# Kernel tuning notes

Hardware: AMD Instinct MI355X
Metric: run time of the kernel (lower is better)

The kernel has to match this reference:

```python
import jax, jax.numpy as jnp
import numpy as np

N_NODES = 100000


def sage_conv(x, src, dst, W_l, b_l, W_r):
    # PyG SAGEConv (aggr='mean'): out = lin_l(mean_{j->i} x_j) + lin_r(x_i)
    # lin_l has bias, lin_r does not.
    msgs = x[src]                                             # [E, d_in] irregular gather
    summed = jax.ops.segment_sum(msgs, dst, num_segments=N_NODES)
    deg = jax.ops.segment_sum(jnp.ones((src.shape[0],), x.dtype), dst,
                              num_segments=N_NODES)
    mean = summed / jnp.maximum(deg, 1.0)[:, None]            # [N, d_in]
    return mean @ W_l.T + b_l + x @ W_r.T                     # [N, d_out]


def setup_inputs() -> dict:
    key = jax.random.key(0)
    ks = jax.random.split(key, 8)
    input_dim, hidden_dim, output_dim = 64, 128, 64
    E = 1600000
    x = jax.random.normal(ks[0], (N_NODES, input_dim), dtype=jnp.float32)
    edge_index = jax.random.randint(ks[1], (2, E), 0, N_NODES, dtype=jnp.int64)

    def glorot(k, shape):
        lim = (6.0 / (shape[0] + shape[1])) ** 0.5
        return jax.random.uniform(k, shape, jnp.float32, -lim, lim)

    W1_l = glorot(ks[2], (hidden_dim, input_dim))
    b1 = jnp.zeros((hidden_dim,), jnp.float32)
    W1_r = glorot(ks[3], (hidden_dim, input_dim))
    W2_l = glorot(ks[4], (output_dim, hidden_dim))
    b2 = jnp.zeros((output_dim,), jnp.float32)
    W2_r = glorot(ks[5], (output_dim, hidden_dim))
    return {"x": x, "edge_index": edge_index,
            "W1_l": W1_l, "b1": b1, "W1_r": W1_r,
            "W2_l": W2_l, "b2": b2, "W2_r": W2_r}


def reference(x, edge_index, W1_l, b1, W1_r, W2_l, b2, W2_r):
    src, dst = edge_index[0], edge_index[1]
    h = jax.nn.relu(sage_conv(x, src, dst, W1_l, b1, W1_r))
    h = jax.nn.relu(sage_conv(h, src, dst, W2_l, b2, W2_r))
    # Original module computes norm(x) and dropout(x) but discards the results,
    # so the returned value is just the second ReLU output.
    return h
```

## Files before the change

kernel.cpp:

```cpp
#include <hip/hip_runtime.h>
#include <hip/hip_bf16.h>


#define NODE_DIM0 64
#define NPBK 256
#define MAXB 512
#define CAPB 5120
#define EPB  4096
#define NSL  16

__device__ inline unsigned short f2bf(float f) {
    unsigned u = __float_as_uint(f);
    return (unsigned short)((u + 0x7fffu + ((u >> 16) & 1u)) >> 16);
}


__global__ __launch_bounds__(256) void bucket_scatter(const int* __restrict__ src,
                                                      const int* __restrict__ dst,
                                                      int* __restrict__ gcur,
                                                      unsigned* __restrict__ pairs, int E) {
    __shared__ int hist[MAXB];
    __shared__ int incl[MAXB];
    __shared__ int exoff[MAXB];
    __shared__ int cur[MAXB];
    __shared__ int chunkBase[MAXB];
    __shared__ unsigned staged[EPB];
    __shared__ unsigned short sbkt[EPB];
    const int t = threadIdx.x;
    const int base = blockIdx.x * EPB;
    int cnt = E - base; if (cnt > EPB) cnt = EPB;

    hist[t] = 0; hist[t + 256] = 0;
    __syncthreads();

    int myS[16], myD[16];
#pragma unroll
    for (int it = 0; it < 16; ++it) {
        int e = base + it * 256 + t;
        if (e < E) {
            myS[it] = src[e];
            myD[it] = dst[e];
            atomicAdd(&hist[myD[it] >> 8], 1);
        } else {
            myD[it] = -1;
        }
    }
    __syncthreads();

    incl[t] = hist[t]; incl[t + 256] = hist[t + 256];
    __syncthreads();
    for (int o = 1; o < MAXB; o <<= 1) {
        int a0 = (t >= o) ? incl[t - o] : 0;
        int a1 = (t + 256 >= o) ? incl[t + 256 - o] : 0;
        __syncthreads();
        incl[t] += a0; incl[t + 256] += a1;
        __syncthreads();
    }
    exoff[t] = incl[t] - hist[t];
    exoff[t + 256] = incl[t + 256] - hist[t + 256];
    cur[t] = 0; cur[t + 256] = 0;
    chunkBase[t] = (hist[t] > 0) ? atomicAdd(&gcur[t], hist[t]) : 0;
    chunkBase[t + 256] = (hist[t + 256] > 0) ? atomicAdd(&gcur[t + 256], hist[t + 256]) : 0;
    __syncthreads();

#pragma unroll
    for (int it = 0; it < 16; ++it) {
        if (myD[it] >= 0) {
            int b = myD[it] >> 8;
            int p = exoff[b] + atomicAdd(&cur[b], 1);
            staged[p] = ((unsigned)(myD[it] & (NPBK - 1)) << 17) | (unsigned)myS[it];
            sbkt[p] = (unsigned short)b;
        }
    }
    __syncthreads();

    for (int p = t; p < cnt; p += 256) {
        int b = sbkt[p];
        int g = chunkBase[b] + (p - exoff[b]);
        if (g < CAPB) pairs[(size_t)b * CAPB + g] = staged[p];
    }
}


__global__ __launch_bounds__(256) void bucket_csr(const unsigned* __restrict__ pairs,
                                                  const int* __restrict__ gcur,
                                                  int* __restrict__ startA,
                                                  int* __restrict__ degA,
                                                  int* __restrict__ esrc, int N) {
    __shared__ int ldeg[NPBK * NSL];
    __shared__ int lcur[NPBK * NSL];
    __shared__ int lsrc[CAPB];
    __shared__ int wsum[256];
    const int b = blockIdx.x;
    const int t = threadIdx.x;
    int cnt = gcur[b]; if (cnt > CAPB) cnt = CAPB;

    for (int i = t; i < NPBK * NSL; i += 256) ldeg[i] = 0;
    __syncthreads();

    const unsigned* reg = pairs + (size_t)b * CAPB;
    for (int i = t; i < cnt; i += 256) {
        unsigned w = reg[i];
        atomicAdd(&ldeg[((w >> 17) << 4) | ((w & 0x1FFFFu) >> 13)], 1);
    }
    __syncthreads();

    const int kbase = t * NSL;
    int run = 0, loc[NSL];
#pragma unroll
    for (int k = 0; k < NSL; ++k) { loc[k] = run; run += ldeg[kbase + k]; }
    wsum[t] = run;
    __syncthreads();
    for (int o = 1; o < 256; o <<= 1) {
        int add = (t >= o) ? wsum[t - o] : 0;
        __syncthreads();
        wsum[t] += add;
        __syncthreads();
    }
    const int excl = wsum[t] - run;
#pragma unroll
    for (int k = 0; k < NSL; ++k) lcur[kbase + k] = excl + loc[k];
    const int node0 = b * NPBK;
    if (node0 + t < N) { startA[node0 + t] = b * CAPB + excl; degA[node0 + t] = run; }
    __syncthreads();

    for (int i = t; i < cnt; i += 256) {
        unsigned w = reg[i];
        int key = (int)((w >> 17) << 4) | (int)((w & 0x1FFFFu) >> 13);
        int pos = atomicAdd(&lcur[key], 1);
        lsrc[pos] = (int)(w & 0x1FFFFu);
    }
    __syncthreads();

    int* outp = esrc + (size_t)b * CAPB;
    for (int i = t; i < cnt; i += 256) outp[i] = lsrc[i];
}


__global__ void cast_bf(const float* __restrict__ in, unsigned short* __restrict__ out,
                        int n4, int* __restrict__ gcur) {
    if (blockIdx.x == 0)
        for (int j = threadIdx.x; j < MAXB; j += 256) gcur[j] = 0;
    int i = blockIdx.x * 256 + threadIdx.x;
    if (i < n4) {
        float4 v = ((const float4*)in)[i];
        ushort4 o;
        o.x = f2bf(v.x); o.y = f2bf(v.y); o.z = f2bf(v.z); o.w = f2bf(v.w);
        ((ushort4*)out)[i] = o;
    }
}

__global__ void cast_weights(const float* __restrict__ a, const float* __restrict__ b,
                             const float* __restrict__ c, const float* __restrict__ d,
                             unsigned short* __restrict__ oa, unsigned short* __restrict__ ob,
                             unsigned short* __restrict__ oc, unsigned short* __restrict__ od) {
    int i = blockIdx.x * 256 + threadIdx.x;
    if (i < 8192) {
        oa[i] = f2bf(a[i]); ob[i] = f2bf(b[i]);
        oc[i] = f2bf(c[i]); od[i] = f2bf(d[i]);
    }
}


template <int MODE>
__global__ __launch_bounds__(256) void gather64(const unsigned short* __restrict__ feat,
                                                const int* __restrict__ startA,
                                                const int* __restrict__ degA,
                                                const int* __restrict__ esrc,
                                                const unsigned short* __restrict__ sdata,
                                                unsigned short* __restrict__ meanOut,
                                                float* __restrict__ outF, int n) {
    const int w = (blockIdx.x * 256 + threadIdx.x) >> 3;
    const int fl = threadIdx.x & 7;
    if (w >= n) return;
    const int s0 = startA[w], dg = degA[w];
    float acc[8] = {0.f, 0.f, 0.f, 0.f, 0.f, 0.f, 0.f, 0.f};
    const int* ep = esrc + s0;
    int e = 0;
    for (; e + 8 <= dg; e += 8) {
        int s_[8];
#pragma unroll
        for (int k = 0; k < 8; ++k) s_[k] = ep[e + k];
        uint4 u[8];
#pragma unroll
        for (int k = 0; k < 8; ++k)
            u[k] = *(const uint4*)(feat + (size_t)s_[k] * 64 + fl * 8);
#pragma unroll
        for (int k = 0; k < 8; ++k) {
            acc[0] += __uint_as_float(u[k].x << 16);
            acc[1] += __uint_as_float(u[k].x & 0xffff0000u);
            acc[2] += __uint_as_float(u[k].y << 16);
            acc[3] += __uint_as_float(u[k].y & 0xffff0000u);
            acc[4] += __uint_as_float(u[k].z << 16);
            acc[5] += __uint_as_float(u[k].z & 0xffff0000u);
            acc[6] += __uint_as_float(u[k].w << 16);
            acc[7] += __uint_as_float(u[k].w & 0xffff0000u);
        }
    }
    for (; e < dg; ++e) {
        uint4 u = *(const uint4*)(feat + (size_t)ep[e] * 64 + fl * 8);
        acc[0] += __uint_as_float(u.x << 16);
        acc[1] += __uint_as_float(u.x & 0xffff0000u);
        acc[2] += __uint_as_float(u.y << 16);
        acc[3] += __uint_as_float(u.y & 0xffff0000u);
        acc[4] += __uint_as_float(u.z << 16);
        acc[5] += __uint_as_float(u.z & 0xffff0000u);
        acc[6] += __uint_as_float(u.w << 16);
        acc[7] += __uint_as_float(u.w & 0xffff0000u);
    }
    const float inv = 1.0f / fmaxf((float)dg, 1.0f);
    if (MODE == 0) {
        unsigned us[8];
#pragma unroll
        for (int q = 0; q < 8; ++q) us[q] = f2bf(acc[q] * inv);
        uint4 o4;
        o4.x = us[0] | (us[1] << 16);
        o4.y = us[2] | (us[3] << 16);
        o4.z = us[4] | (us[5] << 16);
        o4.w = us[6] | (us[7] << 16);
        *(uint4*)(meanOut + (size_t)w * 64 + fl * 8) = o4;
    } else {
        uint4 us = *(const uint4*)(sdata + (size_t)w * 64 + fl * 8);
        float sv8[8];
        sv8[0] = __uint_as_float(us.x << 16);
        sv8[1] = __uint_as_float(us.x & 0xffff0000u);
        sv8[2] = __uint_as_float(us.y << 16);
        sv8[3] = __uint_as_float(us.y & 0xffff0000u);
        sv8[4] = __uint_as_float(us.z << 16);
        sv8[5] = __uint_as_float(us.z & 0xffff0000u);
        sv8[6] = __uint_as_float(us.w << 16);
        sv8[7] = __uint_as_float(us.w & 0xffff0000u);
        float4 o0, o1;
        o0.x = fmaxf(acc[0] * inv + sv8[0], 0.f);
        o0.y = fmaxf(acc[1] * inv + sv8[1], 0.f);
        o0.z = fmaxf(acc[2] * inv + sv8[2], 0.f);
        o0.w = fmaxf(acc[3] * inv + sv8[3], 0.f);
        o1.x = fmaxf(acc[4] * inv + sv8[4], 0.f);
        o1.y = fmaxf(acc[5] * inv + sv8[5], 0.f);
        o1.z = fmaxf(acc[6] * inv + sv8[6], 0.f);
        o1.w = fmaxf(acc[7] * inv + sv8[7], 0.f);
        *(float4*)(outF + (size_t)w * 64 + fl * 8)     = o0;
        *(float4*)(outF + (size_t)w * 64 + fl * 8 + 4) = o1;
    }
}


__global__ __launch_bounds__(256) void fused_l12(const unsigned short* __restrict__ meanb,
                                                 const unsigned short* __restrict__ selfb,
                                                 const unsigned short* __restrict__ W1l,
                                                 const float* __restrict__ b1,
                                                 const unsigned short* __restrict__ W1r,
                                                 const unsigned short* __restrict__ W2l,
                                                 const float* __restrict__ b2,
                                                 const unsigned short* __restrict__ W2r,
                                                 unsigned short* __restrict__ zout,
                                                 unsigned short* __restrict__ sout, int n) {
    using bf16x8 = __attribute__((ext_vector_type(8))) short;
    using f32x4  = __attribute__((ext_vector_type(4))) float;
    constexpr int LDW = 136;
    __shared__ unsigned short h1t[16 * LDW];
    const int wv   = threadIdx.x >> 6;
    const int lane = threadIdx.x & 63;
    const int row16 = lane & 15;
    const int quad  = lane >> 4;

    bf16x8 bl1[2][2], br1[2][2];
    float bv1[2];
#pragma unroll
    for (int r = 0; r < 2; ++r) {
        int nc = (wv * 2 + r) * 16 + row16;
#pragma unroll
        for (int kk = 0; kk < 2; ++kk) {
            bl1[r][kk] = *(const bf16x8*)(W1l + (size_t)nc * 64 + kk * 32 + quad * 8);
            br1[r][kk] = *(const bf16x8*)(W1r + (size_t)nc * 64 + kk * 32 + quad * 8);
        }
        bv1[r] = b1[nc];
    }
    const int nc2 = wv * 16 + row16;
    bf16x8 bl2[4], br2[4];
#pragma unroll
    for (int kk = 0; kk < 4; ++kk) {
        bl2[kk] = *(const bf16x8*)(W2l + (size_t)nc2 * 128 + kk * 32 + quad * 8);
        br2[kk] = *(const bf16x8*)(W2r + (size_t)nc2 * 128 + kk * 32 + quad * 8);
    }
    const float bv2 = b2[nc2];

    const int mtiles = n / 16;
    for (int mt = blockIdx.x; mt < mtiles; mt += gridDim.x) {
        const int m = mt * 16 + row16;
        bf16x8 am[2], as2[2];
#pragma unroll
        for (int kk = 0; kk < 2; ++kk) {
            am[kk]  = *(const bf16x8*)(meanb + (size_t)m * 64 + kk * 32 + quad * 8);
            as2[kk] = *(const bf16x8*)(selfb + (size_t)m * 64 + kk * 32 + quad * 8);
        }
#pragma unroll
        for (int r = 0; r < 2; ++r) {
            f32x4 acc = {0.f, 0.f, 0.f, 0.f};
#pragma unroll
            for (int kk = 0; kk < 2; ++kk)
                acc = __builtin_amdgcn_mfma_f32_16x16x32_bf16(am[kk], bl1[r][kk], acc, 0, 0, 0);
#pragma unroll
            for (int kk = 0; kk < 2; ++kk)
                acc = __builtin_amdgcn_mfma_f32_16x16x32_bf16(as2[kk], br1[r][kk], acc, 0, 0, 0);
            const int nc = (wv * 2 + r) * 16 + row16;
#pragma unroll
            for (int i = 0; i < 4; ++i)
                h1t[(quad * 4 + i) * LDW + nc] = f2bf(fmaxf(acc[i] + bv1[r], 0.f));
        }
        __syncthreads();
        bf16x8 a2[4];
#pragma unroll
        for (int kk = 0; kk < 4; ++kk)
            a2[kk] = *(const bf16x8*)(h1t + row16 * LDW + kk * 32 + quad * 8);
        f32x4 accz = {0.f, 0.f, 0.f, 0.f};
        f32x4 accs = {0.f, 0.f, 0.f, 0.f};
#pragma unroll
        for (int kk = 0; kk < 4; ++kk) {
            accz = __builtin_amdgcn_mfma_f32_16x16x32_bf16(a2[kk], bl2[kk], accz, 0, 0, 0);
            accs = __builtin_amdgcn_mfma_f32_16x16x32_bf16(a2[kk], br2[kk], accs, 0, 0, 0);
        }
        const int rowb = mt * 16 + quad * 4;
#pragma unroll
        for (int i = 0; i < 4; ++i) {
            zout[(size_t)(rowb + i) * 64 + nc2] = f2bf(accz[i]);
            sout[(size_t)(rowb + i) * 64 + nc2] = f2bf(accs[i] + bv2);
        }
        __syncthreads();
    }
}


static inline char* align_up(char* p, size_t a) {
    return (char*)(((uintptr_t)p + a - 1) & ~(uintptr_t)(a - 1));
}

extern "C" void kernel_launch(void* const* d_in, const int* in_sizes, int n_in,
                              void* d_out, int out_size, void* d_ws, size_t ws_size,
                              hipStream_t stream) {
    const float* x   = (const float*)d_in[0];
    const int*   ei  = (const int*)d_in[1];
    const float* W1l = (const float*)d_in[2];
    const float* b1  = (const float*)d_in[3];
    const float* W1r = (const float*)d_in[4];
    const float* W2l = (const float*)d_in[5];
    const float* b2  = (const float*)d_in[6];
    const float* W2r = (const float*)d_in[7];
    float* out = (float*)d_out;

    const int N = in_sizes[0] / NODE_DIM0;
    const int E = in_sizes[1] / 2;
    const int* src = ei;
    const int* dst = ei + E;
    const int nbuck = (N + NPBK - 1) / NPBK;

    char* p = (char*)d_ws;
    int* gcur   = (int*)p; p += (size_t)MAXB * 4;          p = align_up(p, 16);
    int* startA = (int*)p; p += (size_t)N * 4;             p = align_up(p, 16);
    int* degA   = (int*)p; p += (size_t)N * 4;             p = align_up(p, 16);
    int* esrc   = (int*)p; p += (size_t)nbuck * CAPB * 4;  p = align_up(p, 16);
    unsigned short* xbf   = (unsigned short*)p; p += (size_t)N * 64 * 2;
    unsigned short* scr2  = (unsigned short*)p; p += (size_t)N * 128 * 2;
    unsigned short* wl1bf = (unsigned short*)p; p += (size_t)128 * 64 * 2;
    unsigned short* wr1bf = (unsigned short*)p; p += (size_t)128 * 64 * 2;
    unsigned short* wl2bf = (unsigned short*)p; p += (size_t)64 * 128 * 2;
    unsigned short* wr2bf = (unsigned short*)p; p += (size_t)64 * 128 * 2;
    unsigned short* meanbf = (unsigned short*)p; p += (size_t)N * 64 * 2;

    unsigned* pairs = (unsigned*)scr2;
    unsigned short* zbf = scr2;
    unsigned short* sbf = scr2 + (size_t)N * 64;

    cast_bf<<<(N * 64 / 4 + 255) / 256, 256, 0, stream>>>(x, xbf, N * 64 / 4, gcur);

    bucket_scatter<<<(E + EPB - 1) / EPB, 256, 0, stream>>>(src, dst, gcur, pairs, E);
    bucket_csr<<<nbuck, 256, 0, stream>>>(pairs, gcur, startA, degA, esrc, N);

    cast_weights<<<32, 256, 0, stream>>>(W1l, W1r, W2l, W2r, wl1bf, wr1bf, wl2bf, wr2bf);

    gather64<0><<<(N * 8 + 255) / 256, 256, 0, stream>>>(xbf, startA, degA, esrc, nullptr, meanbf, nullptr, N);

    fused_l12<<<1024, 256, 0, stream>>>(meanbf, xbf, wl1bf, b1, wr1bf,
                                        wl2bf, b2, wr2bf, zbf, sbf, N);

    gather64<1><<<(N * 8 + 255) / 256, 256, 0, stream>>>(zbf, startA, degA, esrc, sbf, nullptr, out, N);
}
```

Baseline: 223.5 us.

## Merge cast kernels, widen bucket_scatter to 512 threads, double-buffer fused_l12 LDS

Folds the weight cast into the activation cast kernel, saving one launch. bucket_scatter now runs with 512 threads, so each thread handles 8 edges and the 512-bin histogram scan takes one slot per thread. fused_l12 double-buffers its h1 tile in shared memory and drops the trailing barrier per m-tile. The scatter change raises per-block thread count and may lower occupancy. With two buffers, a fast wave can only run one tile ahead before the next barrier, so the write-after-read hazard should stay covered.

```diff
diff --git a/kernel.cpp b/kernel.cpp
--- a/kernel.cpp
+++ b/kernel.cpp
@@ -15,7 +15,7 @@
 }
 
 
-__global__ __launch_bounds__(256) void bucket_scatter(const int* __restrict__ src,
+__global__ __launch_bounds__(512) void bucket_scatter(const int* __restrict__ src,
                                                       const int* __restrict__ dst,
                                                       int* __restrict__ gcur,
                                                       unsigned* __restrict__ pairs, int E) {
@@ -30,13 +30,13 @@
     const int base = blockIdx.x * EPB;
     int cnt = E - base; if (cnt > EPB) cnt = EPB;
 
-    hist[t] = 0; hist[t + 256] = 0;
-    __syncthreads();
-
-    int myS[16], myD[16];
-#pragma unroll
-    for (int it = 0; it < 16; ++it) {
-        int e = base + it * 256 + t;
+    hist[t] = 0;
+    __syncthreads();
+
+    int myS[8], myD[8];
+#pragma unroll
+    for (int it = 0; it < 8; ++it) {
+        int e = base + it * 512 + t;
         if (e < E) {
             myS[it] = src[e];
             myD[it] = dst[e];
@@ -47,24 +47,21 @@
     }
     __syncthreads();
 
-    incl[t] = hist[t]; incl[t + 256] = hist[t + 256];
+    incl[t] = hist[t];
     __syncthreads();
     for (int o = 1; o < MAXB; o <<= 1) {
         int a0 = (t >= o) ? incl[t - o] : 0;
-        int a1 = (t + 256 >= o) ? incl[t + 256 - o] : 0;
-        __syncthreads();
-        incl[t] += a0; incl[t + 256] += a1;
+        __syncthreads();
+        incl[t] += a0;
         __syncthreads();
     }
     exoff[t] = incl[t] - hist[t];
-    exoff[t + 256] = incl[t + 256] - hist[t + 256];
-    cur[t] = 0; cur[t + 256] = 0;
+    cur[t] = 0;
     chunkBase[t] = (hist[t] > 0) ? atomicAdd(&gcur[t], hist[t]) : 0;
-    chunkBase[t + 256] = (hist[t + 256] > 0) ? atomicAdd(&gcur[t + 256], hist[t + 256]) : 0;
-    __syncthreads();
-
-#pragma unroll
-    for (int it = 0; it < 16; ++it) {
+    __syncthreads();
+
+#pragma unroll
+    for (int it = 0; it < 8; ++it) {
         if (myD[it] >= 0) {
             int b = myD[it] >> 8;
             int p = exoff[b] + atomicAdd(&cur[b], 1);
@@ -74,7 +71,7 @@
     }
     __syncthreads();
 
-    for (int p = t; p < cnt; p += 256) {
+    for (int p = t; p < cnt; p += 512) {
         int b = sbkt[p];
         int g = chunkBase[b] + (p - exoff[b]);
         if (g < CAPB) pairs[(size_t)b * CAPB + g] = staged[p];
@@ -137,25 +134,24 @@
 }
 
 
-__global__ void cast_bf(const float* __restrict__ in, unsigned short* __restrict__ out,
-                        int n4, int* __restrict__ gcur) {
-    if (blockIdx.x == 0)
-        for (int j = threadIdx.x; j < MAXB; j += 256) gcur[j] = 0;
-    int i = blockIdx.x * 256 + threadIdx.x;
-    if (i < n4) {
-        float4 v = ((const float4*)in)[i];
-        ushort4 o;
-        o.x = f2bf(v.x); o.y = f2bf(v.y); o.z = f2bf(v.z); o.w = f2bf(v.w);
-        ((ushort4*)out)[i] = o;
-    }
-}
-
-__global__ void cast_weights(const float* __restrict__ a, const float* __restrict__ b,
-                             const float* __restrict__ c, const float* __restrict__ d,
-                             unsigned short* __restrict__ oa, unsigned short* __restrict__ ob,
-                             unsigned short* __restrict__ oc, unsigned short* __restrict__ od) {
-    int i = blockIdx.x * 256 + threadIdx.x;
-    if (i < 8192) {
+__global__ void cast_all(const float* __restrict__ in, unsigned short* __restrict__ out,
+                         int n4, int cblk, int* __restrict__ gcur,
+                         const float* __restrict__ a, const float* __restrict__ b,
+                         const float* __restrict__ c, const float* __restrict__ d,
+                         unsigned short* __restrict__ oa, unsigned short* __restrict__ ob,
+                         unsigned short* __restrict__ oc, unsigned short* __restrict__ od) {
+    if (blockIdx.x < (unsigned)cblk) {
+        if (blockIdx.x == 0)
+            for (int j = threadIdx.x; j < MAXB; j += 256) gcur[j] = 0;
+        int i = blockIdx.x * 256 + threadIdx.x;
+        if (i < n4) {
+            float4 v = ((const float4*)in)[i];
+            ushort4 o;
+            o.x = f2bf(v.x); o.y = f2bf(v.y); o.z = f2bf(v.z); o.w = f2bf(v.w);
+            ((ushort4*)out)[i] = o;
+        }
+    } else {
+        int i = (blockIdx.x - cblk) * 256 + threadIdx.x;
         oa[i] = f2bf(a[i]); ob[i] = f2bf(b[i]);
         oc[i] = f2bf(c[i]); od[i] = f2bf(d[i]);
     }
@@ -258,7 +254,7 @@
     using bf16x8 = __attribute__((ext_vector_type(8))) short;
     using f32x4  = __attribute__((ext_vector_type(4))) float;
     constexpr int LDW = 136;
-    __shared__ unsigned short h1t[16 * LDW];
+    __shared__ unsigned short h1t[2][16 * LDW];
     const int wv   = threadIdx.x >> 6;
     const int lane = threadIdx.x & 63;
     const int row16 = lane & 15;
@@ -286,6 +282,7 @@
     const float bv2 = b2[nc2];
 
     const int mtiles = n / 16;
+    int pb = 0;
     for (int mt = blockIdx.x; mt < mtiles; mt += gridDim.x) {
         const int m = mt * 16 + row16;
         bf16x8 am[2], as2[2];
@@ -306,13 +303,13 @@
             const int nc = (wv * 2 + r) * 16 + row16;
 #pragma unroll
             for (int i = 0; i < 4; ++i)
-                h1t[(quad * 4 + i) * LDW + nc] = f2bf(fmaxf(acc[i] + bv1[r], 0.f));
+                h1t[pb][(quad * 4 + i) * LDW + nc] = f2bf(fmaxf(acc[i] + bv1[r], 0.f));
         }
         __syncthreads();
         bf16x8 a2[4];
 #pragma unroll
         for (int kk = 0; kk < 4; ++kk)
-            a2[kk] = *(const bf16x8*)(h1t + row16 * LDW + kk * 32 + quad * 8);
+            a2[kk] = *(const bf16x8*)(h1t[pb] + row16 * LDW + kk * 32 + quad * 8);
         f32x4 accz = {0.f, 0.f, 0.f, 0.f};
         f32x4 accs = {0.f, 0.f, 0.f, 0.f};
 #pragma unroll
@@ -326,7 +323,7 @@
             zout[(size_t)(rowb + i) * 64 + nc2] = f2bf(accz[i]);
             sout[(size_t)(rowb + i) * 64 + nc2] = f2bf(accs[i] + bv2);
         }
-        __syncthreads();
+        pb ^= 1;
     }
 }
 
@@ -371,12 +368,13 @@
     unsigned short* zbf = scr2;
     unsigned short* sbf = scr2 + (size_t)N * 64;
 
-    cast_bf<<<(N * 64 / 4 + 255) / 256, 256, 0, stream>>>(x, xbf, N * 64 / 4, gcur);
-
-    bucket_scatter<<<(E + EPB - 1) / EPB, 256, 0, stream>>>(src, dst, gcur, pairs, E);
+    const int cblk = (N * 64 / 4 + 255) / 256;
+    cast_all<<<cblk + 32, 256, 0, stream>>>(x, xbf, N * 64 / 4, cblk, gcur,
+                                            W1l, W1r, W2l, W2r,
+                                            wl1bf, wr1bf, wl2bf, wr2bf);
+
+    bucket_scatter<<<(E + EPB - 1) / EPB, 512, 0, stream>>>(src, dst, gcur, pairs, E);
     bucket_csr<<<nbuck, 256, 0, stream>>>(pairs, gcur, startA, degA, esrc, N);
-
-    cast_weights<<<32, 256, 0, stream>>>(W1l, W1r, W2l, W2r, wl1bf, wr1bf, wl2bf, wr2bf);
 
     gather64<0><<<(N * 8 + 255) / 256, 256, 0, stream>>>(xbf, startA, degA, esrc, nullptr, meanbf, nullptr, N);
 
```

After: 217.4 us (median of 2 runs). 2.7% less time.
